# Optimization experiments

Hardware: AMD Instinct MI355X
Metric: run time of the kernel (lower is better)

Reference implementation:

```python
import sys
import jax, jax.numpy as jnp
import numpy as np

sys.setrecursionlimit(100000)

MARGIN = 200.0
SAME_MARGIN = 0.0
REL_MARGIN = MARGIN - SAME_MARGIN  # margin - same_margin


def km_algorithm(mp):
    """Faithful numpy port of the repo's recursive Kuhn-Munkres (host-side,
    exactly mirroring the original CPU round-trip). mp: (n, n) float64.
    Returns transport plan T with T[link[y], y] = 1/n for matched pairs."""
    n = mp.shape[0]
    link = np.full(n, -1, dtype=np.int64)
    lx = mp.max(axis=1).astype(np.float64).copy()
    ly = np.zeros(n, dtype=np.float64)
    st = {}

    def dfs(x):
        st['visx'][x] = True
        for y in range(n):
            if st['visy'][y]:
                continue
            tmp = lx[x] + ly[y] - mp[x, y]
            if abs(tmp) < 1e-5:
                st['visy'][y] = True
                if link[y] == -1 or dfs(link[y]):
                    link[y] = x
                    return True
            elif st['sla'][y] + 1e-5 > tmp:
                st['sla'][y] = tmp
        return False

    for x in range(n):
        st['sla'] = np.full(n, 1e10, dtype=np.float64)
        while True:
            st['visx'] = np.zeros(n, dtype=bool)
            st['visy'] = np.zeros(n, dtype=bool)
            if dfs(x):
                break
            d = st['sla'][~st['visy']].min()
            lx[st['visx']] -= d
            ly[st['visy']] += d
            st['sla'][~st['visy']] -= d
    T = np.zeros((n, n), dtype=np.float64)
    for i in range(n):
        if link[i] != -1:
            T[link[i], i] = 1.0 / n
    return T


def sim_label(l1, l2):
    # (n, n) float: 1 where labels equal
    return (l1[:, None] == l2[None, :]).astype(jnp.float32)


def ground_metric(f1, f2, sim):
    # pairwise squared euclidean distances: ||a||^2 - 2 a.b + ||b||^2
    sq1 = jnp.sum(f1 * f1, axis=1)[:, None]
    sq2 = jnp.sum(f2 * f2, axis=1)[None, :]
    d2 = sq1 - 2.0 * (f1 @ f2.T) + sq2
    hinge_gm = jnp.maximum(0.0, SAME_MARGIN + REL_MARGIN - d2)   # negative pairs
    same_gm = jnp.maximum(0.0, d2 - SAME_MARGIN)                 # positive pairs
    return sim * same_gm + (1.0 - sim) * hinge_gm                # mode='both'


def setup_inputs() -> dict:
    key = jax.random.key(0)
    k1, k2, k3, k4 = jax.random.split(key, 4)
    n, d = 128, 8192
    return {
        "inputs_batch1": jax.random.normal(k1, (n, d), dtype=jnp.float32),
        "inputs_batch2": jax.random.normal(k2, (n, d), dtype=jnp.float32),
        "targets_batch1": jax.random.randint(k3, (n,), 0, 16, dtype=jnp.int64) if jax.config.jax_enable_x64 else jax.random.randint(k3, (n,), 0, 16).astype(jnp.int32),
        "targets_batch2": jax.random.randint(k4, (n,), 0, 16, dtype=jnp.int64) if jax.config.jax_enable_x64 else jax.random.randint(k4, (n,), 0, 16).astype(jnp.int32),
    }


def reference(inputs_batch1, inputs_batch2, targets_batch1, targets_batch2):
    sim = sim_label(targets_batch1, targets_batch2)
    GM = ground_metric(inputs_batch1, inputs_batch2, sim)
    # host round-trip for KM assignment, as in the original module
    T = km_algorithm(np.asarray(jax.device_get(GM), dtype=np.float64))
    T = jnp.asarray(T, dtype=jnp.float32)
    loss = jnp.sum(GM * T)
    return loss
```

## Files before the change

kernel.cpp:

```cpp
#include <hip/hip_runtime.h>

#define N 128
#define DIM 8192
#define NN (N * N)
#define ZSPLIT 64
#define NW 16
#define GSTRIDE 130

__device__ __forceinline__ void wave_fence() {
    __threadfence_block();
    __builtin_amdgcn_wave_barrier();
}
__device__ __forceinline__ double embed_key(double v, int j) {
    long long b = __double_as_longlong(v);
    return __longlong_as_double((b & ~127LL) | (long long)j);
}

__global__ __launch_bounds__(256) void d2_partial(const float* __restrict__ A,
                                                  const float* __restrict__ B,
                                                  float* __restrict__ d2p) {
    __shared__ float As[32][68];
    __shared__ float Bk[64][36];
    const int tid = threadIdx.x;
    const int bi = blockIdx.x, bj = blockIdx.y, bz = blockIdx.z;
    const int tx = tid & 15, ty = tid >> 4;
    const int row0 = bi * 32, col0 = bj * 32;
    const int kbase = bz * 128;
    float a00 = 0.f, a01 = 0.f, a10 = 0.f, a11 = 0.f;

    for (int it = 0; it < 2; ++it) {
        const int k0 = kbase + it * 64;
        __syncthreads();
        #pragma unroll
        for (int s = 0; s < 2; ++s) {
            int e = tid + s * 256;
            int r = e >> 4, q = e & 15;
            *(float4*)&As[r][q * 4] = *(const float4*)&A[(row0 + r) * DIM + k0 + q * 4];
        }
        #pragma unroll
        for (int s = 0; s < 2; ++s) {
            int r = tid & 31;
            int kq = (tid >> 5) + s * 8;
            float4 b4 = *(const float4*)&B[(col0 + r) * DIM + k0 + kq * 4];
            Bk[kq * 4 + 0][r] = b4.x;
            Bk[kq * 4 + 1][r] = b4.y;
            Bk[kq * 4 + 2][r] = b4.z;
            Bk[kq * 4 + 3][r] = b4.w;
        }
        __syncthreads();
        #pragma unroll
        for (int kk = 0; kk < 64; kk += 4) {
            float x0[4], x1[4];
            *(float4*)x0 = *(const float4*)&As[2 * ty][kk];
            *(float4*)x1 = *(const float4*)&As[2 * ty + 1][kk];
            float y[4][2];
            #pragma unroll
            for (int q = 0; q < 4; ++q)
                *(float2*)y[q] = *(const float2*)&Bk[kk + q][2 * tx];
            #pragma unroll
            for (int q = 0; q < 4; ++q) {
                float d;
                d = x0[q] - y[q][0]; a00 = fmaf(d, d, a00);
                d = x0[q] - y[q][1]; a01 = fmaf(d, d, a01);
                d = x1[q] - y[q][0]; a10 = fmaf(d, d, a10);
                d = x1[q] - y[q][1]; a11 = fmaf(d, d, a11);
            }
        }
    }
    const int o0 = (row0 + 2 * ty) * N + col0 + 2 * tx;
    float* dst = d2p + bz * NN;
    *(float2*)&dst[o0]     = make_float2(a00, a01);
    *(float2*)&dst[o0 + N] = make_float2(a10, a11);
}

__global__ __launch_bounds__(256) void reduce_gm(const float* __restrict__ d2p,
                                                 const int* __restrict__ t1,
                                                 const int* __restrict__ t2,
                                                 float* __restrict__ gm,
                                                 int* __restrict__ flagarr) {
    __shared__ int bf;
    if (threadIdx.x == 0) bf = 0;
    __syncthreads();
    const int o = blockIdx.x * 256 + threadIdx.x;
    float s0 = 0.f, s1 = 0.f, s2 = 0.f, s3 = 0.f, s4 = 0.f, s5 = 0.f, s6 = 0.f, s7 = 0.f;
    const float* p = d2p + o;
    #pragma unroll
    for (int z = 0; z < ZSPLIT; z += 8) {
        s0 += p[(z + 0) * NN]; s1 += p[(z + 1) * NN];
        s2 += p[(z + 2) * NN]; s3 += p[(z + 3) * NN];
        s4 += p[(z + 4) * NN]; s5 += p[(z + 5) * NN];
        s6 += p[(z + 6) * NN]; s7 += p[(z + 7) * NN];
    }
    float s = ((s0 + s1) + (s2 + s3)) + ((s4 + s5) + (s6 + s7));
    const int i = o >> 7, j = o & 127;
    const int l1 = t1[i], l2 = t2[j];
    const bool same = (l1 == l2);
    float g = same ? fmaxf(s, 0.f) : fmaxf(200.f - s, 0.f);
    gm[o] = g;
    bool bad = (!same && g > 0.f) || l1 < 0 || l1 > 63 || l2 < 0 || l2 > 63;
    unsigned long long m = __ballot(bad);
    if ((threadIdx.x & 63) == 0 && m) atomicOr(&bf, 1);
    __syncthreads();
    if (threadIdx.x == 0) flagarr[blockIdx.x] = bf;
}

__global__ __launch_bounds__(1024) void solve_kernel(const float* __restrict__ gm,
                                                     const int* __restrict__ flagarr,
                                                     const int* __restrict__ t1,
                                                     const int* __restrict__ t2,
                                                     float* __restrict__ out) {
    __shared__ float gml[N * GSTRIDE];
    __shared__ int lbl1[N], lbl2[N];
    __shared__ int rowlist[N], collist[N];
    __shared__ int rcnt[64], ccnt[64], rstart[65], cstart[65], rcur[64], ccur[64];
    __shared__ int tasks[65], bigtasks[65];
    __shared__ int ntasks_s, nbig_s, flag_s;
    __shared__ double totals[NW];
    __shared__ int claimw[NW][64];
    __shared__ double ub[N + 1], vbp[N + 1], minvb[N + 1];
    __shared__ int pb[N + 1], wayb[N + 1], usedb[N + 1];
    __shared__ double redv[NW];
    __shared__ int redi[NW];
    __shared__ double big_total;
    __shared__ int jfin_s;

    const int tid = threadIdx.x;
    if (tid < 64) { rcnt[tid] = 0; ccnt[tid] = 0; rcur[tid] = 0; ccur[tid] = 0; }
    if (tid == 0) { ntasks_s = 0; nbig_s = 0; flag_s = 0; big_total = 0.0; }
    if (tid < N)  { lbl1[tid] = t1[tid]; lbl2[tid] = t2[tid]; }
    __syncthreads();
    if (tid < 64 && flagarr[tid]) atomicOr(&flag_s, 1);
    if (tid < N) {
        atomicAdd(&rcnt[lbl1[tid] & 63], 1);
        atomicAdd(&ccnt[lbl2[tid] & 63], 1);
    }
    __syncthreads();
    if (tid < 64) {
        int rs_ = rcnt[tid], cs_ = ccnt[tid];
        #pragma unroll
        for (int o = 1; o < 64; o <<= 1) {
            int tr = __shfl_up(rs_, o, 64);
            int tc = __shfl_up(cs_, o, 64);
            if (tid >= o) { rs_ += tr; cs_ += tc; }
        }
        rstart[tid + 1] = rs_;
        cstart[tid + 1] = cs_;
        if (tid == 0) { rstart[0] = 0; cstart[0] = 0; }
        if (!flag_s) {
            int R = rcnt[tid], C = ccnt[tid];
            bool valid = (R > 0) && (C > 0);
            bool small = valid && (R <= 64) && (C <= 64);
            bool big   = valid && !small;
            unsigned long long ms = __ballot(small);
            unsigned long long mb = __ballot(big);
            if (small) tasks[__popcll(ms & ((1ull << tid) - 1))] = tid;
            if (big)   bigtasks[__popcll(mb & ((1ull << tid) - 1))] = tid;
            if (tid == 0) { ntasks_s = __popcll(ms); nbig_s = __popcll(mb); }
        } else if (tid == 0) { ntasks_s = 0; nbig_s = 1; bigtasks[0] = -1; }
    }
    __syncthreads();
    if (tid < N) {
        int l1 = lbl1[tid] & 63;
        int p = atomicAdd(&rcur[l1], 1);
        rowlist[rstart[l1] + p] = tid;
        int l2 = lbl2[tid] & 63;
        int q = atomicAdd(&ccur[l2], 1);
        collist[cstart[l2] + q] = tid;
    }
    __syncthreads();
    #pragma unroll
    for (int pch = 0; pch < 16; ++pch) {
        int e = tid + pch * 1024;
        int i = e >> 7, j = e & 127;
        gml[i * GSTRIDE + j] = gm[rowlist[i] * N + collist[j]];
    }
    __syncthreads();

    const int w = tid >> 6, lane = tid & 63;
    const int ntasks = ntasks_s;
    double acc = 0.0;

    for (int tk = w; tk < ntasks; tk += NW) {
        const int c = tasks[tk];
        const int Rn = rcnt[c], Cn = ccnt[c], rs = rstart[c], cs = cstart[c];
        const bool T  = (Rn > Cn);
        const int n_  = T ? Cn : Rn;
        const int m_  = T ? Rn : Cn;
        const int rstep = T ? 1 : GSTRIDE;
        const int cstep = T ? GSTRIDE : 1;
        const int rb00 = T ? cs : rs * GSTRIDE;
        const int ob00 = T ? rs * GSTRIDE : cs;
        int* clm = claimw[w];

        const bool cA = (lane < m_), rA = (lane < n_);
        const int myoff = ob00 + lane * cstep;
        const int myrb  = rb00 + lane * rstep;

        double u = 0.0;
        if (rA) {
            float mx = 0.f;
            int a = myrb + ob00;
            for (int j = 0; j < m_; ++j) { mx = fmaxf(mx, gml[a]); a += cstep; }
            u = -(double)mx;
        }
        double v = 1e30;
        {
            int a = rb00 + myoff;
            for (int i = 0; i < n_; ++i) {
                double ui = __shfl(u, i, 64);
                if (cA) v = fmin(v, -(double)gml[a] - ui);
                a += rstep;
            }
        }
        if (cA) clm[lane] = 0x7fffffff;
        wave_fence();
        int jc = -1;
        {
            int a = myrb + ob00;
            for (int j = 0; j < m_; ++j) {
                double vj = __shfl(v, j, 64);
                if (rA && jc < 0) {
                    double s = -(double)gml[a] - u - vj;
                    if (s < 1e-7) jc = j;
                }
                a += cstep;
            }
        }
        if (rA && jc >= 0) atomicMin(&clm[jc], lane);
        wave_fence();
        int p = -1;
        if (cA && clm[lane] != 0x7fffffff) p = clm[lane];
        bool rowm = (rA && jc >= 0 && clm[jc] == lane);

        for (int ir = 0; ir < n_; ++ir) {
            if (__shfl(rowm ? 1 : 0, ir, 64)) continue;
            double minv = 1e30, markD = -1.0, ent = -1.0;
            bool used = false; int way = -2;
            if (rA && lane == ir) ent = 0.0;
            double D = 0.0;
            int i0 = ir, jprev = -1;
            int guard = 2 * m_ + 8;
            while (guard-- > 0) {
                double ui = __shfl(u, i0, 64);
                int rb = rb00 + i0 * rstep;
                if (cA && !used) {
                    double cand = D - ui - (double)gml[rb + myoff] - v;
                    if (cand < minv) { minv = cand; way = jprev; }
                }
                double kd = (cA && !used) ? embed_key(minv, lane) : 1e30;
                #pragma unroll
                for (int o = 1; o < 64; o <<= 1) kd = fmin(kd, __shfl_xor(kd, o, 64));
                long long kb = __double_as_longlong(kd);
                int j1 = (int)(kb & 127);
                double Dn = __longlong_as_double(kb & ~127LL);
                if (Dn > 1e29) break;
                D = Dn;
                int i1 = __shfl(p, j1, 64);
                if (i1 < 0) {
                    int jj = j1;
                    while (true) {
                        int wp = __shfl(way, jj, 64);
                        int pn = (wp < 0) ? ir : __shfl(p, wp, 64);
                        if (cA && lane == jj) p = pn;
                        if (wp < 0) break;
                        jj = wp;
                    }
                    if (rA && lane == ir) rowm = true;
                    break;
                }
                if (cA && lane == j1) { used = true; markD = D; }
                if (rA && lane == i1) ent = D;
                jprev = j1; i0 = i1;
            }
            if (rA && ent   >= 0.0) u += D - ent;
            if (cA && markD >= 0.0) v -= D - markD;
        }

        double val = 0.0;
        if (cA && p >= 0) val = (double)gml[rb00 + p * rstep + myoff];
        #pragma unroll
        for (int o = 1; o < 64; o <<= 1) val += __shfl_xor(val, o, 64);
        acc += val;
    }
    if (lane == 0) totals[w] = acc;
    __syncthreads();

    const int nbig = nbig_s;
    for (int bt = 0; bt < nbig; ++bt) {
        const int c = bigtasks[bt];
        int Rn, Cn, rs, cs;
        if (c < 0) { Rn = N; Cn = N; rs = 0; cs = 0; }
        else { Rn = rcnt[c]; Cn = ccnt[c]; rs = rstart[c]; cs = cstart[c]; }
        const bool T = (Rn > Cn);
        const int n_ = T ? Cn : Rn, m_ = T ? Rn : Cn;
        const int rstep = T ? 1 : GSTRIDE;
        const int cstep = T ? GSTRIDE : 1;
        const int rb00 = T ? cs : rs * GSTRIDE;
        const int ob00 = T ? rs * GSTRIDE : cs;
        auto cost = [&](int i, int j) -> double {
            return -(double)gml[rb00 + i * rstep + ob00 + j * cstep];
        };
        for (int x = tid; x <= m_; x += 1024) { vbp[x] = 0.0; pb[x] = 0; }
        for (int x = tid; x <= n_; x += 1024) { ub[x] = 0.0; }
        __syncthreads();
        for (int i = 1; i <= n_; ++i) {
            if (tid == 0) pb[0] = i;
            for (int x = tid; x <= m_; x += 1024) { minvb[x] = 1e300; usedb[x] = 0; }
            __syncthreads();
            int j0 = 0;
            int guard = 2 * m_ + 8;
            while (guard-- > 0) {
                if (tid == 0) usedb[j0] = 1;
                __syncthreads();
                const int i0 = pb[j0];
                double dl = 1e300; int jl = 0;
                if (tid < m_) {
                    int j = tid + 1;
                    if (!usedb[j]) {
                        double cur = cost(i0 - 1, j - 1) - ub[i0] - vbp[j];
                        if (cur < minvb[j]) { minvb[j] = cur; wayb[j] = j0; }
                        dl = minvb[j]; jl = j;
                    }
                }
                double rv = dl; int ri = jl;
                #pragma unroll
                for (int o = 32; o > 0; o >>= 1) {
                    double ov = __shfl_down(rv, o, 64);
                    int oi2 = __shfl_down(ri, o, 64);
                    if (ov < rv) { rv = ov; ri = oi2; }
                }
                if ((tid & 63) == 0) { redv[tid >> 6] = rv; redi[tid >> 6] = ri; }
                __syncthreads();
                if (tid == 0) {
                    double bd = 1e300; int bj = 0;
                    for (int q = 0; q < NW; ++q) if (redv[q] < bd) { bd = redv[q]; bj = redi[q]; }
                    redv[0] = bd; redi[0] = bj;
                }
                __syncthreads();
                const double delta = redv[0];
                const int j1 = redi[0];
                if (tid < m_) {
                    int j = tid + 1;
                    if (usedb[j]) { ub[pb[j]] += delta; vbp[j] -= delta; }
                    else          { minvb[j] -= delta; }
                }
                if (tid == 0) ub[pb[0]] += delta;
                __syncthreads();
                j0 = j1;
                if (pb[j0] == 0) break;
            }
            if (tid == 0) jfin_s = j0;
            __syncthreads();
            if (tid == 0) {
                int jj = jfin_s;
                while (jj) { int jp = wayb[jj]; pb[jj] = pb[jp]; jj = jp; }
            }
            __syncthreads();
        }
        double bl = 0.0;
        if (tid < m_) { int j = tid + 1; if (pb[j] != 0) bl = -cost(pb[j] - 1, j - 1); }
        #pragma unroll
        for (int o = 32; o > 0; o >>= 1) bl += __shfl_down(bl, o, 64);
        if ((tid & 63) == 0) redv[tid >> 6] = bl;
        __syncthreads();
        if (tid == 0) { double s = 0; for (int q = 0; q < NW; ++q) s += redv[q]; big_total += s; }
        __syncthreads();
    }

    if (tid == 0) {
        double s = big_total;
        for (int i = 0; i < NW; ++i) s += totals[i];
        out[0] = (float)(s / (double)N);
    }
}

extern "C" void kernel_launch(void* const* d_in, const int* in_sizes, int n_in,
                              void* d_out, int out_size, void* d_ws, size_t ws_size,
                              hipStream_t stream) {
    const float* A  = (const float*)d_in[0];
    const float* B  = (const float*)d_in[1];
    const int*   t1 = (const int*)d_in[2];
    const int*   t2 = (const int*)d_in[3];
    float* out = (float*)d_out;
    float* d2p = (float*)d_ws;
    float* gm  = (float*)d_ws + ZSPLIT * NN;
    int*   flagarr = (int*)(gm + NN);

    d2_partial<<<dim3(4, 4, ZSPLIT), 256, 0, stream>>>(A, B, d2p);
    reduce_gm<<<64, 256, 0, stream>>>(d2p, t1, t2, gm, flagarr);
    solve_kernel<<<1, 1024, 0, stream>>>(gm, flagarr, t1, t2, out);
}
```

Measured before the change: 92.69 us.

## Split per-class assignment solves across 64 blocks with a separate finalize kernel

The per-label-class Hungarian solves, which previously ran on 16 waves of a single 1024-thread block, now run one class per 64-thread block across 64 blocks. Each block gathers only its own class submatrix into LDS. The wave-min reduction width is cut to the next power of two above the class size. A new finalize kernel sums the per-class results and handles the large or fallback cases, and it skips the full matrix gather when there are none. This trades an extra kernel launch and a global round trip for spreading the serial work across compute units.

```diff
diff --git a/kernel.cpp b/kernel.cpp
--- a/kernel.cpp
+++ b/kernel.cpp
@@ -6,6 +6,7 @@
 #define ZSPLIT 64
 #define NW 16
 #define GSTRIDE 130
+#define NSTR 65
 
 __device__ __forceinline__ void wave_fence() {
     __threadfence_block();
@@ -104,29 +105,169 @@
     if (threadIdx.x == 0) flagarr[blockIdx.x] = bf;
 }
 
-__global__ __launch_bounds__(1024) void solve_kernel(const float* __restrict__ gm,
-                                                     const int* __restrict__ flagarr,
-                                                     const int* __restrict__ t1,
-                                                     const int* __restrict__ t2,
-                                                     float* __restrict__ out) {
+__global__ __launch_bounds__(64) void solve_classes(const float* __restrict__ gm,
+                                                    const int* __restrict__ flagarr,
+                                                    const int* __restrict__ t1,
+                                                    const int* __restrict__ t2,
+                                                    double* __restrict__ cls_val) {
+    __shared__ float ncls[64 * NSTR];
+    __shared__ int rowl[64], coll[64];
+    __shared__ int rcnt[64], ccnt[64];
+    __shared__ int tasks[64];
+    __shared__ int clm[64];
+
+    const int lane = threadIdx.x;
+    const int l1a = t1[lane] & 63, l1b = t1[lane + 64] & 63;
+    const int l2a = t2[lane] & 63, l2b = t2[lane + 64] & 63;
+    const int fl  = flagarr[lane];
+    rcnt[lane] = 0; ccnt[lane] = 0;
+    __syncthreads();
+    atomicAdd(&rcnt[l1a], 1); atomicAdd(&rcnt[l1b], 1);
+    atomicAdd(&ccnt[l2a], 1); atomicAdd(&ccnt[l2b], 1);
+    __syncthreads();
+    const bool flag = (__ballot(fl != 0) != 0ull);
+    int ntasks;
+    {
+        int R = rcnt[lane], C = ccnt[lane];
+        bool small = (!flag) && (R > 0) && (C > 0) && (R <= 64) && (C <= 64);
+        unsigned long long ms = __ballot(small);
+        if (small) tasks[__popcll(ms & ((1ull << lane) - 1))] = lane;
+        ntasks = (int)__popcll(ms);
+    }
+    __syncthreads();
+    if ((int)blockIdx.x >= ntasks) {
+        if (lane == 0) cls_val[blockIdx.x] = 0.0;
+        return;
+    }
+    const int c = tasks[blockIdx.x];
+
+    const unsigned long long mlt = (1ull << lane) - 1;
+    unsigned long long b1 = __ballot(l1a == c);
+    unsigned long long b2 = __ballot(l1b == c);
+    if (l1a == c) rowl[__popcll(b1 & mlt)] = lane;
+    if (l1b == c) rowl[__popcll(b1) + __popcll(b2 & mlt)] = lane + 64;
+    const int Rn = (int)(__popcll(b1) + __popcll(b2));
+    unsigned long long c1 = __ballot(l2a == c);
+    unsigned long long c2 = __ballot(l2b == c);
+    if (l2a == c) coll[__popcll(c1 & mlt)] = lane;
+    if (l2b == c) coll[__popcll(c1) + __popcll(c2 & mlt)] = lane + 64;
+    const int Cn = (int)(__popcll(c1) + __popcll(c2));
+    __syncthreads();
+
+    const bool T  = (Rn > Cn);
+    const int n_  = T ? Cn : Rn;
+    const int m_  = T ? Rn : Cn;
+    const int tot = n_ * m_;
+    for (int e = lane; e < tot; e += 64) {
+        int i = e / m_, j = e - i * m_;
+        int gr = T ? rowl[j] : rowl[i];
+        int gc = T ? coll[i] : coll[j];
+        ncls[i * NSTR + j] = gm[gr * N + gc];
+    }
+    __syncthreads();
+
+    const int W = (m_ <= 16) ? 16 : (m_ <= 32 ? 32 : 64);
+    const bool cA = (lane < m_), rA = (lane < n_);
+
+    double u = 0.0;
+    if (rA) {
+        float mx = 0.f;
+        const float* row = &ncls[lane * NSTR];
+        for (int j = 0; j < m_; ++j) mx = fmaxf(mx, row[j]);
+        u = -(double)mx;
+    }
+    double v = 1e30;
+    for (int i = 0; i < n_; ++i) {
+        double ui = __shfl(u, i, 64);
+        if (cA) v = fmin(v, -(double)ncls[i * NSTR + lane] - ui);
+    }
+    if (cA) clm[lane] = 0x7fffffff;
+    wave_fence();
+    int jc = -1;
+    for (int j = 0; j < m_; ++j) {
+        double vj = __shfl(v, j, 64);
+        if (rA && jc < 0) {
+            double s = -(double)ncls[lane * NSTR + j] - u - vj;
+            if (s < 1e-7) jc = j;
+        }
+    }
+    if (rA && jc >= 0) atomicMin(&clm[jc], lane);
+    wave_fence();
+    int p = -1;
+    if (cA && clm[lane] != 0x7fffffff) p = clm[lane];
+    bool rowm = (rA && jc >= 0 && clm[jc] == lane);
+
+    for (int ir = 0; ir < n_; ++ir) {
+        if (__shfl(rowm ? 1 : 0, ir, 64)) continue;
+        double minv = 1e30, markD = -1.0, ent = -1.0;
+        bool used = false; int way = -2;
+        if (rA && lane == ir) ent = 0.0;
+        double D = 0.0;
+        int i0 = ir, jprev = -1;
+        int guard = 2 * m_ + 8;
+        while (guard-- > 0) {
+            double ui = __shfl(u, i0, 64);
+            if (cA && !used) {
+                double cand = D - ui - (double)ncls[i0 * NSTR + lane] - v;
+                if (cand < minv) { minv = cand; way = jprev; }
+            }
+            double kd = (cA && !used) ? embed_key(minv, lane) : 1e30;
+            for (int o = 1; o < W; o <<= 1) kd = fmin(kd, __shfl_xor(kd, o, 64));
+            long long kb = __double_as_longlong(kd);
+            int j1 = (int)(kb & 127);
+            double Dn = __longlong_as_double(kb & ~127LL);
+            if (Dn > 1e29) break;
+            D = Dn;
+            int i1 = __shfl(p, j1, 64);
+            if (i1 < 0) {
+                int jj = j1;
+                while (true) {
+                    int wp = __shfl(way, jj, 64);
+                    int pn = (wp < 0) ? ir : __shfl(p, wp, 64);
+                    if (cA && lane == jj) p = pn;
+                    if (wp < 0) break;
+                    jj = wp;
+                }
+                if (rA && lane == ir) rowm = true;
+                break;
+            }
+            if (cA && lane == j1) { used = true; markD = D; }
+            if (rA && lane == i1) ent = D;
+            jprev = j1; i0 = i1;
+        }
+        if (rA && ent   >= 0.0) u += D - ent;
+        if (cA && markD >= 0.0) v -= D - markD;
+    }
+
+    double val = 0.0;
+    if (cA && p >= 0) val = (double)ncls[p * NSTR + lane];
+    #pragma unroll
+    for (int o = 1; o < 64; o <<= 1) val += __shfl_xor(val, o, 64);
+    if (lane == 0) cls_val[blockIdx.x] = val;
+}
+
+__global__ __launch_bounds__(1024) void finalize_kernel(const float* __restrict__ gm,
+                                                        const int* __restrict__ flagarr,
+                                                        const int* __restrict__ t1,
+                                                        const int* __restrict__ t2,
+                                                        const double* __restrict__ cls_val,
+                                                        float* __restrict__ out) {
     __shared__ float gml[N * GSTRIDE];
     __shared__ int lbl1[N], lbl2[N];
     __shared__ int rowlist[N], collist[N];
     __shared__ int rcnt[64], ccnt[64], rstart[65], cstart[65], rcur[64], ccur[64];
-    __shared__ int tasks[65], bigtasks[65];
-    __shared__ int ntasks_s, nbig_s, flag_s;
-    __shared__ double totals[NW];
-    __shared__ int claimw[NW][64];
+    __shared__ int bigtasks[65];
+    __shared__ int nbig_s, flag_s;
     __shared__ double ub[N + 1], vbp[N + 1], minvb[N + 1];
     __shared__ int pb[N + 1], wayb[N + 1], usedb[N + 1];
     __shared__ double redv[NW];
     __shared__ int redi[NW];
-    __shared__ double big_total;
+    __shared__ double big_total, small_sum;
     __shared__ int jfin_s;
 
     const int tid = threadIdx.x;
     if (tid < 64) { rcnt[tid] = 0; ccnt[tid] = 0; rcur[tid] = 0; ccur[tid] = 0; }
-    if (tid == 0) { ntasks_s = 0; nbig_s = 0; flag_s = 0; big_total = 0.0; }
+    if (tid == 0) { nbig_s = 0; flag_s = 0; big_total = 0.0; }
     if (tid < N)  { lbl1[tid] = t1[tid]; lbl2[tid] = t2[tid]; }
     __syncthreads();
     if (tid < 64 && flagarr[tid]) atomicOr(&flag_s, 1);
@@ -134,6 +275,7 @@
         atomicAdd(&rcnt[lbl1[tid] & 63], 1);
         atomicAdd(&ccnt[lbl2[tid] & 63], 1);
     }
+    double sv = (tid < 64) ? cls_val[tid] : 0.0;
     __syncthreads();
     if (tid < 64) {
         int rs_ = rcnt[tid], cs_ = ccnt[tid];
@@ -148,230 +290,119 @@
         if (tid == 0) { rstart[0] = 0; cstart[0] = 0; }
         if (!flag_s) {
             int R = rcnt[tid], C = ccnt[tid];
-            bool valid = (R > 0) && (C > 0);
-            bool small = valid && (R <= 64) && (C <= 64);
-            bool big   = valid && !small;
-            unsigned long long ms = __ballot(small);
+            bool big = (R > 0) && (C > 0) && ((R > 64) || (C > 64));
             unsigned long long mb = __ballot(big);
-            if (small) tasks[__popcll(ms & ((1ull << tid) - 1))] = tid;
-            if (big)   bigtasks[__popcll(mb & ((1ull << tid) - 1))] = tid;
-            if (tid == 0) { ntasks_s = __popcll(ms); nbig_s = __popcll(mb); }
-        } else if (tid == 0) { ntasks_s = 0; nbig_s = 1; bigtasks[0] = -1; }
-    }
-    __syncthreads();
-    if (tid < N) {
-        int l1 = lbl1[tid] & 63;
-        int p = atomicAdd(&rcur[l1], 1);
-        rowlist[rstart[l1] + p] = tid;
-        int l2 = lbl2[tid] & 63;
-        int q = atomicAdd(&ccur[l2], 1);
-        collist[cstart[l2] + q] = tid;
-    }
-    __syncthreads();
-    #pragma unroll
-    for (int pch = 0; pch < 16; ++pch) {
-        int e = tid + pch * 1024;
-        int i = e >> 7, j = e & 127;
-        gml[i * GSTRIDE + j] = gm[rowlist[i] * N + collist[j]];
-    }
-    __syncthreads();
-
-    const int w = tid >> 6, lane = tid & 63;
-    const int ntasks = ntasks_s;
-    double acc = 0.0;
-
-    for (int tk = w; tk < ntasks; tk += NW) {
-        const int c = tasks[tk];
-        const int Rn = rcnt[c], Cn = ccnt[c], rs = rstart[c], cs = cstart[c];
-        const bool T  = (Rn > Cn);
-        const int n_  = T ? Cn : Rn;
-        const int m_  = T ? Rn : Cn;
-        const int rstep = T ? 1 : GSTRIDE;
-        const int cstep = T ? GSTRIDE : 1;
-        const int rb00 = T ? cs : rs * GSTRIDE;
-        const int ob00 = T ? rs * GSTRIDE : cs;
-        int* clm = claimw[w];
-
-        const bool cA = (lane < m_), rA = (lane < n_);
-        const int myoff = ob00 + lane * cstep;
-        const int myrb  = rb00 + lane * rstep;
-
-        double u = 0.0;
-        if (rA) {
-            float mx = 0.f;
-            int a = myrb + ob00;
-            for (int j = 0; j < m_; ++j) { mx = fmaxf(mx, gml[a]); a += cstep; }
-            u = -(double)mx;
-        }
-        double v = 1e30;
-        {
-            int a = rb00 + myoff;
-            for (int i = 0; i < n_; ++i) {
-                double ui = __shfl(u, i, 64);
-                if (cA) v = fmin(v, -(double)gml[a] - ui);
-                a += rstep;
-            }
-        }
-        if (cA) clm[lane] = 0x7fffffff;
-        wave_fence();
-        int jc = -1;
-        {
-            int a = myrb + ob00;
-            for (int j = 0; j < m_; ++j) {
-                double vj = __shfl(v, j, 64);
-                if (rA && jc < 0) {
-                    double s = -(double)gml[a] - u - vj;
-                    if (s < 1e-7) jc = j;
+            if (big) bigtasks[__popcll(mb & ((1ull << tid) - 1))] = tid;
+            if (tid == 0) nbig_s = __popcll(mb);
+        } else if (tid == 0) { nbig_s = 1; bigtasks[0] = -1; }
+        #pragma unroll
+        for (int o = 1; o < 64; o <<= 1) sv += __shfl_xor(sv, o, 64);
+        if (tid == 0) small_sum = sv;
+    }
+    __syncthreads();
+
+    const int nbig = nbig_s;
+    if (nbig > 0) {
+        if (tid < N) {
+            int l1 = lbl1[tid] & 63;
+            int p = atomicAdd(&rcur[l1], 1);
+            rowlist[rstart[l1] + p] = tid;
+            int l2 = lbl2[tid] & 63;
+            int q = atomicAdd(&ccur[l2], 1);
+            collist[cstart[l2] + q] = tid;
+        }
+        __syncthreads();
+        #pragma unroll
+        for (int pch = 0; pch < 16; ++pch) {
+            int e = tid + pch * 1024;
+            int i = e >> 7, j = e & 127;
+            gml[i * GSTRIDE + j] = gm[rowlist[i] * N + collist[j]];
+        }
+        __syncthreads();
+
+        for (int bt = 0; bt < nbig; ++bt) {
+            const int c = bigtasks[bt];
+            int Rn, Cn, rs, cs;
+            if (c < 0) { Rn = N; Cn = N; rs = 0; cs = 0; }
+            else { Rn = rcnt[c]; Cn = ccnt[c]; rs = rstart[c]; cs = cstart[c]; }
+            const bool T = (Rn > Cn);
+            const int n_ = T ? Cn : Rn, m_ = T ? Rn : Cn;
+            const int rstep = T ? 1 : GSTRIDE;
+            const int cstep = T ? GSTRIDE : 1;
+            const int rb00 = T ? cs : rs * GSTRIDE;
+            const int ob00 = T ? rs * GSTRIDE : cs;
+            auto cost = [&](int i, int j) -> double {
+                return -(double)gml[rb00 + i * rstep + ob00 + j * cstep];
+            };
+            for (int x = tid; x <= m_; x += 1024) { vbp[x] = 0.0; pb[x] = 0; }
+            for (int x = tid; x <= n_; x += 1024) { ub[x] = 0.0; }
+            __syncthreads();
+            for (int i = 1; i <= n_; ++i) {
+                if (tid == 0) pb[0] = i;
+                for (int x = tid; x <= m_; x += 1024) { minvb[x] = 1e300; usedb[x] = 0; }
+                __syncthreads();
+                int j0 = 0;
+                int guard = 2 * m_ + 8;
+                while (guard-- > 0) {
+                    if (tid == 0) usedb[j0] = 1;
+                    __syncthreads();
+                    const int i0 = pb[j0];
+                    double dl = 1e300; int jl = 0;
+                    if (tid < m_) {
+                        int j = tid + 1;
+                        if (!usedb[j]) {
+                            double cur = cost(i0 - 1, j - 1) - ub[i0] - vbp[j];
+                            if (cur < minvb[j]) { minvb[j] = cur; wayb[j] = j0; }
+                            dl = minvb[j]; jl = j;
+                        }
+                    }
+                    double rv = dl; int ri = jl;
+                    #pragma unroll
+                    for (int o = 32; o > 0; o >>= 1) {
+                        double ov = __shfl_down(rv, o, 64);
+                        int oi2 = __shfl_down(ri, o, 64);
+                        if (ov < rv) { rv = ov; ri = oi2; }
+                    }
+                    if ((tid & 63) == 0) { redv[tid >> 6] = rv; redi[tid >> 6] = ri; }
+                    __syncthreads();
+                    if (tid == 0) {
+                        double bd = 1e300; int bj = 0;
+                        for (int q = 0; q < NW; ++q) if (redv[q] < bd) { bd = redv[q]; bj = redi[q]; }
+                        redv[0] = bd; redi[0] = bj;
+                    }
+                    __syncthreads();
+                    const double delta = redv[0];
+                    const int j1 = redi[0];
+                    if (tid < m_) {
+                        int j = tid + 1;
+                        if (usedb[j]) { ub[pb[j]] += delta; vbp[j] -= delta; }
+                        else          { minvb[j] -= delta; }
+                    }
+                    if (tid == 0) ub[pb[0]] += delta;
+                    __syncthreads();
+                    j0 = j1;
+                    if (pb[j0] == 0) break;
                 }
-                a += cstep;
-            }
-        }
-        if (rA && jc >= 0) atomicMin(&clm[jc], lane);
-        wave_fence();
-        int p = -1;
-        if (cA && clm[lane] != 0x7fffffff) p = clm[lane];
-        bool rowm = (rA && jc >= 0 && clm[jc] == lane);
-
-        for (int ir = 0; ir < n_; ++ir) {
-            if (__shfl(rowm ? 1 : 0, ir, 64)) continue;
-            double minv = 1e30, markD = -1.0, ent = -1.0;
-            bool used = false; int way = -2;
-            if (rA && lane == ir) ent = 0.0;
-            double D = 0.0;
-            int i0 = ir, jprev = -1;
-            int guard = 2 * m_ + 8;
-            while (guard-- > 0) {
-                double ui = __shfl(u, i0, 64);
-                int rb = rb00 + i0 * rstep;
-                if (cA && !used) {
-                    double cand = D - ui - (double)gml[rb + myoff] - v;
-                    if (cand < minv) { minv = cand; way = jprev; }
-                }
-                double kd = (cA && !used) ? embed_key(minv, lane) : 1e30;
-                #pragma unroll
-                for (int o = 1; o < 64; o <<= 1) kd = fmin(kd, __shfl_xor(kd, o, 64));
-                long long kb = __double_as_longlong(kd);
-                int j1 = (int)(kb & 127);
-                double Dn = __longlong_as_double(kb & ~127LL);
-                if (Dn > 1e29) break;
-                D = Dn;
-                int i1 = __shfl(p, j1, 64);
-                if (i1 < 0) {
-                    int jj = j1;
-                    while (true) {
-                        int wp = __shfl(way, jj, 64);
-                        int pn = (wp < 0) ? ir : __shfl(p, wp, 64);
-                        if (cA && lane == jj) p = pn;
-                        if (wp < 0) break;
-                        jj = wp;
-                    }
-                    if (rA && lane == ir) rowm = true;
-                    break;
-                }
-                if (cA && lane == j1) { used = true; markD = D; }
-                if (rA && lane == i1) ent = D;
-                jprev = j1; i0 = i1;
-            }
-            if (rA && ent   >= 0.0) u += D - ent;
-            if (cA && markD >= 0.0) v -= D - markD;
-        }
-
-        double val = 0.0;
-        if (cA && p >= 0) val = (double)gml[rb00 + p * rstep + myoff];
-        #pragma unroll
-        for (int o = 1; o < 64; o <<= 1) val += __shfl_xor(val, o, 64);
-        acc += val;
-    }
-    if (lane == 0) totals[w] = acc;
-    __syncthreads();
-
-    const int nbig = nbig_s;
-    for (int bt = 0; bt < nbig; ++bt) {
-        const int c = bigtasks[bt];
-        int Rn, Cn, rs, cs;
-        if (c < 0) { Rn = N; Cn = N; rs = 0; cs = 0; }
-        else { Rn = rcnt[c]; Cn = ccnt[c]; rs = rstart[c]; cs = cstart[c]; }
-        const bool T = (Rn > Cn);
-        const int n_ = T ? Cn : Rn, m_ = T ? Rn : Cn;
-        const int rstep = T ? 1 : GSTRIDE;
-        const int cstep = T ? GSTRIDE : 1;
-        const int rb00 = T ? cs : rs * GSTRIDE;
-        const int ob00 = T ? rs * GSTRIDE : cs;
-        auto cost = [&](int i, int j) -> double {
-            return -(double)gml[rb00 + i * rstep + ob00 + j * cstep];
-        };
-        for (int x = tid; x <= m_; x += 1024) { vbp[x] = 0.0; pb[x] = 0; }
-        for (int x = tid; x <= n_; x += 1024) { ub[x] = 0.0; }
-        __syncthreads();
-        for (int i = 1; i <= n_; ++i) {
-            if (tid == 0) pb[0] = i;
-            for (int x = tid; x <= m_; x += 1024) { minvb[x] = 1e300; usedb[x] = 0; }
-            __syncthreads();
-            int j0 = 0;
-            int guard = 2 * m_ + 8;
-            while (guard-- > 0) {
-                if (tid == 0) usedb[j0] = 1;
-                __syncthreads();
-                const int i0 = pb[j0];
-                double dl = 1e300; int jl = 0;
-                if (tid < m_) {
-                    int j = tid + 1;
-                    if (!usedb[j]) {
-                        double cur = cost(i0 - 1, j - 1) - ub[i0] - vbp[j];
-                        if (cur < minvb[j]) { minvb[j] = cur; wayb[j] = j0; }
-                        dl = minvb[j]; jl = j;
-                    }
-                }
-                double rv = dl; int ri = jl;
-                #pragma unroll
-                for (int o = 32; o > 0; o >>= 1) {
-                    double ov = __shfl_down(rv, o, 64);
-                    int oi2 = __shfl_down(ri, o, 64);
-                    if (ov < rv) { rv = ov; ri = oi2; }
-                }
-                if ((tid & 63) == 0) { redv[tid >> 6] = rv; redi[tid >> 6] = ri; }
+                if (tid == 0) jfin_s = j0;
                 __syncthreads();
                 if (tid == 0) {
-                    double bd = 1e300; int bj = 0;
-                    for (int q = 0; q < NW; ++q) if (redv[q] < bd) { bd = redv[q]; bj = redi[q]; }
-                    redv[0] = bd; redi[0] = bj;
+                    int jj = jfin_s;
+                    while (jj) { int jp = wayb[jj]; pb[jj] = pb[jp]; jj = jp; }
                 }
                 __syncthreads();
-                const double delta = redv[0];
-                const int j1 = redi[0];
-                if (tid < m_) {
-                    int j = tid + 1;
-                    if (usedb[j]) { ub[pb[j]] += delta; vbp[j] -= delta; }
-                    else          { minvb[j] -= delta; }
-                }
-                if (tid == 0) ub[pb[0]] += delta;
-                __syncthreads();
-                j0 = j1;
-                if (pb[j0] == 0) break;
             }
-            if (tid == 0) jfin_s = j0;
+            double bl = 0.0;
+            if (tid < m_) { int j = tid + 1; if (pb[j] != 0) bl = -cost(pb[j] - 1, j - 1); }
+            #pragma unroll
+            for (int o = 32; o > 0; o >>= 1) bl += __shfl_down(bl, o, 64);
+            if ((tid & 63) == 0) redv[tid >> 6] = bl;
             __syncthreads();
-            if (tid == 0) {
-                int jj = jfin_s;
-                while (jj) { int jp = wayb[jj]; pb[jj] = pb[jp]; jj = jp; }
-            }
+            if (tid == 0) { double s = 0; for (int q = 0; q < NW; ++q) s += redv[q]; big_total += s; }
             __syncthreads();
         }
-        double bl = 0.0;
-        if (tid < m_) { int j = tid + 1; if (pb[j] != 0) bl = -cost(pb[j] - 1, j - 1); }
-        #pragma unroll
-        for (int o = 32; o > 0; o >>= 1) bl += __shfl_down(bl, o, 64);
-        if ((tid & 63) == 0) redv[tid >> 6] = bl;
-        __syncthreads();
-        if (tid == 0) { double s = 0; for (int q = 0; q < NW; ++q) s += redv[q]; big_total += s; }
-        __syncthreads();
-    }
-
-    if (tid == 0) {
-        double s = big_total;
-        for (int i = 0; i < NW; ++i) s += totals[i];
-        out[0] = (float)(s / (double)N);
-    }
+    }
+
+    if (tid == 0) out[0] = (float)((small_sum + big_total) / (double)N);
 }
 
 extern "C" void kernel_launch(void* const* d_in, const int* in_sizes, int n_in,
@@ -385,8 +416,10 @@
     float* d2p = (float*)d_ws;
     float* gm  = (float*)d_ws + ZSPLIT * NN;
     int*   flagarr = (int*)(gm + NN);
+    double* cls_val = (double*)(flagarr + 64);
 
     d2_partial<<<dim3(4, 4, ZSPLIT), 256, 0, stream>>>(A, B, d2p);
     reduce_gm<<<64, 256, 0, stream>>>(d2p, t1, t2, gm, flagarr);
-    solve_kernel<<<1, 1024, 0, stream>>>(gm, flagarr, t1, t2, out);
-}
+    solve_classes<<<64, 64, 0, stream>>>(gm, flagarr, t1, t2, cls_val);
+    finalize_kernel<<<1, 1024, 0, stream>>>(gm, flagarr, t1, t2, cls_val, out);
+}
```

Measured after the change: 88.80 us. 4.2% less time.
